# Performance work log

Measured on AMD Instinct MI355X. Metric: run time of the kernel, lower is better.

## Reference

```python
import jax, jax.numpy as jnp
import numpy as np

MAX_DIST = 32.0
GRID_RES = 0.5
BOX = int(np.ceil(2 * MAX_DIST / GRID_RES + 1))  # 129


def setup_inputs() -> dict:
    key = jax.random.key(0)
    k1, k2 = jax.random.split(key)
    B, N, F = 1, 500000, 32
    # scale so most points are inside the [-32, 32] box, some outside
    coords = jax.random.normal(k1, (B, N, 3), dtype=jnp.float32) * 20.0
    features = jax.random.normal(k2, (B, N, F), dtype=jnp.float32)
    return {"coords": coords, "features": features}


def reference(coords, features):
    B, N, _ = coords.shape
    F = features.shape[2]
    # voxel indices
    gc = jnp.round((coords + MAX_DIST) / GRID_RES).astype(jnp.int32)  # (B,N,3)
    in_box = jnp.all((gc >= 0) & (gc < BOX), axis=-1)                 # (B,N)
    # instead of boolean_mask (dynamic shape), zero out-of-box features and
    # clamp their indices; scatter-add of zeros is a no-op, matching
    # tf.scatter_nd's duplicate-summing semantics on the masked set.
    feats = jnp.where(in_box[..., None], features, jnp.zeros((), features.dtype))
    gcc = jnp.clip(gc, 0, BOX - 1)
    b_idx = jnp.broadcast_to(jnp.arange(B)[:, None], (B, N))
    grid = jnp.zeros((B, BOX, BOX, BOX, F), dtype=features.dtype)
    grid = grid.at[b_idx, gcc[..., 0], gcc[..., 1], gcc[..., 2]].add(feats)
    return grid
```

## Files before the change

### kernel.cpp

```cpp
#include <hip/hip_runtime.h>
#include <hip/hip_bf16.h>

#define MAX_DIST 32.0f
#define BOX 129

__global__ void __launch_bounds__(256) scatter_kernel(
    const float* __restrict__ coords,
    const float* __restrict__ features,
    float* __restrict__ grid,
    int N) {
  int total = N * 32;
  int stride = gridDim.x * blockDim.x;
  for (int t = blockIdx.x * blockDim.x + threadIdx.x; t < total; t += stride) {
    int p = t >> 5;
    int f = t & 31;
    float x = coords[3 * p + 0];
    float y = coords[3 * p + 1];
    float z = coords[3 * p + 2];
    int gx = __float2int_rn((x + MAX_DIST) * 2.0f);
    int gy = __float2int_rn((y + MAX_DIST) * 2.0f);
    int gz = __float2int_rn((z + MAX_DIST) * 2.0f);
    if ((unsigned)gx < BOX && (unsigned)gy < BOX && (unsigned)gz < BOX) {
      long cell = ((long)gx * BOX + gy) * BOX + gz;
      atomicAdd(&grid[cell * 32 + f], features[(long)p * 32 + f]);
    }
  }
}

extern "C" void kernel_launch(void* const* d_in, const int* in_sizes, int n_in,
                              void* d_out, int out_size, void* d_ws, size_t ws_size,
                              hipStream_t stream) {
  const float* coords   = (const float*)d_in[0];
  const float* features = (const float*)d_in[1];
  float* grid = (float*)d_out;

  int N = in_sizes[0] / 3;

  hipMemsetAsync(d_out, 0, (size_t)out_size * sizeof(float), stream);

  int total = N * 32;
  int block = 256;
  int grid_blocks = 4096;
  if (grid_blocks > (total + block - 1) / block)
    grid_blocks = (total + block - 1) / block;
  scatter_kernel<<<grid_blocks, block, 0, stream>>>(coords, features, grid, N);
}
```

Before: 356.2 us.

## Replace atomic scatter-add with per-cell linked lists and a gather pass

The per-feature global atomicAdd scatter is replaced by two kernels. The first builds a linked list of points per voxel cell with atomicExch on a head array in workspace. The second walks each cell's list and writes the summed features with float4 stores, which also removes the separate zeroing memset of the large output grid. This only runs when the workspace can hold the head and next arrays; otherwise a float2-loaded atomic fallback runs. Summation order now differs from the atomic version, and long lists cause pointer-chasing latency in dense cells.

After: 374.2 us. 1.05x slower.

```diff
diff --git a/kernel.cpp b/kernel.cpp
--- a/kernel.cpp
+++ b/kernel.cpp
@@ -3,17 +3,15 @@
 
 #define MAX_DIST 32.0f
 #define BOX 129
+#define BOX3 (129 * 129 * 129)
 
-__global__ void __launch_bounds__(256) scatter_kernel(
+__global__ void __launch_bounds__(256) build_lists_kernel(
     const float* __restrict__ coords,
-    const float* __restrict__ features,
-    float* __restrict__ grid,
+    int* __restrict__ head,
+    int* __restrict__ next,
     int N) {
-  int total = N * 32;
   int stride = gridDim.x * blockDim.x;
-  for (int t = blockIdx.x * blockDim.x + threadIdx.x; t < total; t += stride) {
-    int p = t >> 5;
-    int f = t & 31;
+  for (int p = blockIdx.x * blockDim.x + threadIdx.x; p < N; p += stride) {
     float x = coords[3 * p + 0];
     float y = coords[3 * p + 1];
     float z = coords[3 * p + 2];
@@ -21,8 +19,52 @@
     int gy = __float2int_rn((y + MAX_DIST) * 2.0f);
     int gz = __float2int_rn((z + MAX_DIST) * 2.0f);
     if ((unsigned)gx < BOX && (unsigned)gy < BOX && (unsigned)gz < BOX) {
-      long cell = ((long)gx * BOX + gy) * BOX + gz;
-      atomicAdd(&grid[cell * 32 + f], features[(long)p * 32 + f]);
+      int cell = (gx * BOX + gy) * BOX + gz;
+      next[p] = atomicExch(&head[cell], p);
+    }
+  }
+}
+
+__global__ void __launch_bounds__(256) gather_kernel(
+    const int* __restrict__ head,
+    const int* __restrict__ next,
+    const float4* __restrict__ feats4,
+    float4* __restrict__ grid4) {
+  long t = (long)blockIdx.x * blockDim.x + threadIdx.x;
+  if (t >= (long)BOX3 * 8) return;
+  int cell = (int)(t >> 3);
+  int fp = (int)(t & 7);
+  float4 acc = make_float4(0.f, 0.f, 0.f, 0.f);
+  int p = head[cell];
+  while (p >= 0) {
+    float4 v = feats4[(long)p * 8 + fp];
+    acc.x += v.x; acc.y += v.y; acc.z += v.z; acc.w += v.w;
+    p = next[p];
+  }
+  grid4[t] = acc;
+}
+
+__global__ void __launch_bounds__(256) scatter_fallback_kernel(
+    const float* __restrict__ coords,
+    const float2* __restrict__ feats,
+    float* __restrict__ grid,
+    int N) {
+  int total = N * 16;
+  int stride = gridDim.x * blockDim.x;
+  for (int t = blockIdx.x * blockDim.x + threadIdx.x; t < total; t += stride) {
+    int p = t >> 4;
+    int fp = t & 15;
+    float x = coords[3 * p + 0];
+    float y = coords[3 * p + 1];
+    float z = coords[3 * p + 2];
+    int gx = __float2int_rn((x + MAX_DIST) * 2.0f);
+    int gy = __float2int_rn((y + MAX_DIST) * 2.0f);
+    int gz = __float2int_rn((z + MAX_DIST) * 2.0f);
+    if ((unsigned)gx < BOX && (unsigned)gy < BOX && (unsigned)gz < BOX) {
+      float2 v = feats[(long)p * 16 + fp];
+      long base = (((long)gx * BOX + gy) * BOX + gz) * 32 + 2 * fp;
+      atomicAdd(&grid[base + 0], v.x);
+      atomicAdd(&grid[base + 1], v.y);
     }
   }
 }
@@ -30,18 +72,32 @@
 extern "C" void kernel_launch(void* const* d_in, const int* in_sizes, int n_in,
                               void* d_out, int out_size, void* d_ws, size_t ws_size,
                               hipStream_t stream) {
-  const float* coords   = (const float*)d_in[0];
-  const float* features = (const float*)d_in[1];
-  float* grid = (float*)d_out;
-
+  const float* coords = (const float*)d_in[0];
   int N = in_sizes[0] / 3;
 
-  hipMemsetAsync(d_out, 0, (size_t)out_size * sizeof(float), stream);
+  size_t head_bytes = (size_t)BOX3 * sizeof(int);
+  size_t head_pad   = (head_bytes + 255) & ~(size_t)255;
+  size_t needed     = head_pad + (size_t)N * sizeof(int);
 
-  int total = N * 32;
-  int block = 256;
-  int grid_blocks = 4096;
-  if (grid_blocks > (total + block - 1) / block)
-    grid_blocks = (total + block - 1) / block;
-  scatter_kernel<<<grid_blocks, block, 0, stream>>>(coords, features, grid, N);
+  if (ws_size >= needed) {
+    int* head = (int*)d_ws;
+    int* next = (int*)((char*)d_ws + head_pad);
+
+    hipMemsetAsync(head, 0xFF, head_bytes, stream);
+
+    int blocks2 = (N + 255) / 256;
+    build_lists_kernel<<<blocks2, 256, 0, stream>>>(coords, head, next, N);
+
+    long total3 = (long)BOX3 * 8;
+    int blocks3 = (int)((total3 + 255) / 256);
+    gather_kernel<<<blocks3, 256, 0, stream>>>(
+        head, next, (const float4*)d_in[1], (float4*)d_out);
+  } else {
+    hipMemsetAsync(d_out, 0, (size_t)out_size * sizeof(float), stream);
+    int total = N * 16;
+    int blocks = 4096;
+    if (blocks > (total + 255) / 256) blocks = (total + 255) / 256;
+    scatter_fallback_kernel<<<blocks, 256, 0, stream>>>(
+        coords, (const float2*)d_in[1], (float*)d_out, N);
+  }
 }
```
